# Optimization experiments

Measured on AMD Instinct MI355X. Metric: run time of the kernel, lower is better.

Reference implementation:

```python
import jax, jax.numpy as jnp
import numpy as np
import math

D_MODEL = 1024
EXPAND = 2
D_INNER = D_MODEL * EXPAND          # 2048
D_STATE = 16
NHEADS = 8
NGROUPS = 1
D_CONV = 4
HEADDIM = D_INNER // NHEADS         # 256
CONV_DIM = D_INNER + 2 * NGROUPS * D_STATE   # x, B, C go through the causal conv
D_IN_PROJ = 2 * D_INNER + 2 * NGROUPS * D_STATE + NHEADS  # z, xBC, dt
CHUNK = 64
BATCH = 4
SEQLEN = 4096


def setup_inputs() -> dict:
    key = jax.random.key(0)
    ks = jax.random.split(key, 6)
    rng = np.random.default_rng(0)
    u = jax.random.normal(ks[0], (BATCH, SEQLEN, D_MODEL), dtype=jnp.float32)
    W_in = jax.random.normal(ks[1], (D_MODEL, D_IN_PROJ), dtype=jnp.float32) * 0.02
    conv_w = jax.random.normal(ks[2], (CONV_DIM, D_CONV), dtype=jnp.float32) * (1.0 / math.sqrt(D_CONV))
    conv_b = jnp.zeros((CONV_DIM,), dtype=jnp.float32)
    # dt_bias = inverse-softplus of dt sampled log-uniform in [dt_min, dt_max]
    dt = np.exp(rng.uniform(size=NHEADS) * (math.log(0.1) - math.log(0.001)) + math.log(0.001))
    dt = np.clip(dt, 1e-4, None)
    dt_bias = jnp.asarray(dt + np.log(-np.expm1(-dt)), dtype=jnp.float32)
    # A in A_init_range=(0.9, 0.999), stored as A_log with A = -exp(A_log)
    A_log = jnp.asarray(np.log(rng.uniform(0.9, 0.999, NHEADS)), dtype=jnp.float32)
    D = jnp.ones((NHEADS,), dtype=jnp.float32)
    norm_w = jnp.ones((D_INNER,), dtype=jnp.float32)
    W_out = jax.random.normal(ks[3], (D_INNER, D_MODEL), dtype=jnp.float32) * 0.02
    return {"u": u, "W_in": W_in, "conv_w": conv_w, "conv_b": conv_b,
            "dt_bias": dt_bias, "A_log": A_log, "D": D, "norm_w": norm_w, "W_out": W_out}


def _mamba2_fwd(u, W_in, conv_w, conv_b, dt_bias, A_log, D, norm_w, W_out):
    b, l, _ = u.shape
    h, p, n, g, Q = NHEADS, HEADDIM, D_STATE, NGROUPS, CHUNK
    zxbcdt = u @ W_in                                   # [b,l,2*d_inner+2gn+h]
    z = zxbcdt[..., :D_INNER]
    xBC = zxbcdt[..., D_INNER:D_INNER + CONV_DIM]
    dt = jax.nn.softplus(zxbcdt[..., D_INNER + CONV_DIM:] + dt_bias)  # [b,l,h]
    # causal depthwise conv over time (d_conv taps) + SiLU
    xp = jnp.pad(xBC, ((0, 0), (D_CONV - 1, 0), (0, 0)))
    xconv = conv_b
    for k in range(D_CONV):
        xconv = xconv + xp[:, k:k + l, :] * conv_w[:, k]
    xBC = jax.nn.silu(xconv)
    x = xBC[..., :D_INNER].reshape(b, l, h, p)
    B = xBC[..., D_INNER:D_INNER + g * n].reshape(b, l, g, n)
    C = xBC[..., D_INNER + g * n:].reshape(b, l, g, n)
    Bh = jnp.repeat(B, h // g, axis=2)                  # [b,l,h,n]
    Ch = jnp.repeat(C, h // g, axis=2)
    A = -jnp.exp(A_log)                                 # [h]
    # ---- chunked (SSD) selective scan ----
    nc = l // Q
    xc = x.reshape(b, nc, Q, h, p)
    dtc = dt.reshape(b, nc, Q, h)
    Bc = Bh.reshape(b, nc, Q, h, n)
    Cc = Ch.reshape(b, nc, Q, h, n)
    a = dtc * A                                         # [b,nc,Q,h]
    cs = jnp.cumsum(a, axis=2).transpose(0, 1, 3, 2)    # [b,nc,h,Q]
    mask = jnp.tril(jnp.ones((Q, Q), dtype=bool))
    L = jnp.where(mask, jnp.exp(cs[..., :, None] - cs[..., None, :]), 0.0)  # [b,nc,h,Q,Q]
    xdt = xc * dtc[..., None]                           # x scaled by dt
    Y_diag = jnp.einsum('bcqhn,bcshn,bchqs,bcshp->bcqhp', Cc, Bc, L, xdt)
    decay_states = jnp.exp(cs[..., -1:] - cs)           # [b,nc,h,Q]
    states = jnp.einsum('bcqhn,bchq,bcqhp->bchpn', Bc, decay_states, xdt)  # per-chunk state
    chunk_decay = jnp.exp(cs[..., -1])                  # [b,nc,h]
    def step(carry, inp):
        st, dec = inp
        new = dec[..., None, None] * carry + st
        return new, carry
    init = jnp.zeros((b, h, p, n), dtype=u.dtype)
    _, prev = jax.lax.scan(step, init, (states.transpose(1, 0, 2, 3, 4), chunk_decay.transpose(1, 0, 2)))
    prev = prev.transpose(1, 0, 2, 3, 4)                # state entering each chunk [b,nc,h,p,n]
    Y_off = jnp.einsum('bcqhn,bchpn,bchq->bcqhp', Cc, prev, jnp.exp(cs))
    y = (Y_diag + Y_off).reshape(b, l, h, p) + D[:, None] * x
    y = y.reshape(b, l, D_INNER)
    # gated RMSNorm then out projection
    y = y * jax.nn.silu(z)
    y = y * jax.lax.rsqrt(jnp.mean(y * y, axis=-1, keepdims=True) + 1e-5) * norm_w
    return y @ W_out


def reference(u, W_in, conv_w, conv_b, dt_bias, A_log, D, norm_w, W_out):
    return _mamba2_fwd(u, W_in, conv_w, conv_b, dt_bias, A_log, D, norm_w, W_out)
```

## Files before the change

kernel.cpp:

```cpp
#include <hip/hip_runtime.h>
#include <cstddef>
#include <cstdint>
#include <type_traits>

constexpr int DM = 1024;
constexpr int DI = 2048;
constexpr int DS = 16;
constexpr int NH = 8;
constexpr int CD = 2080;
constexpr int DP = 4136;
constexpr int DPT = 4224;
constexpr int Q  = 64;
constexpr int B_ = 4;
constexpr int L_ = 4096;
constexpr int NCH = 64;
constexpr int HP = 256;
constexpr int NR = B_ * L_;

constexpr size_t AL(size_t x) { return (x + 255) & ~(size_t)255; }
constexpr size_t OFFB_ZX = 0;
constexpr size_t OFFB_BC = AL(OFFB_ZX + (size_t)NR * DP * 2);
constexpr size_t OFFB_DT = AL(OFFB_BC + (size_t)NR * 32 * 4);
constexpr size_t OFFB_CS = AL(OFFB_DT + (size_t)NR * NH * 4);
constexpr size_t OFFB_ST = AL(OFFB_CS + (size_t)B_ * NCH * NH * Q * 4);
constexpr size_t OFFB_Y  = AL(OFFB_ST + (size_t)B_ * NCH * NH * HP * DS * 4);
constexpr size_t OFFB_WO = AL(OFFB_Y + (size_t)NR * DI * 2);

__device__ __forceinline__ float silu_f(float x) { return x / (1.f + expf(-x)); }
__device__ __forceinline__ float bf2f(unsigned short v) {
  unsigned int u = ((unsigned int)v) << 16;
  return __builtin_bit_cast(float, u);
}
__device__ __forceinline__ unsigned short f2bf(float f) {
  unsigned int u = __builtin_bit_cast(unsigned int, f);
  u += 0x7FFFu + ((u >> 16) & 1u);
  return (unsigned short)(u >> 16);
}

typedef __attribute__((ext_vector_type(8))) short bf16x8;
typedef __attribute__((ext_vector_type(4))) float f32x4;

template<bool OUT_BF16>
__global__ __launch_bounds__(256)
void gemm_mfma(const unsigned short* __restrict__ A, const unsigned short* __restrict__ Bt,
               void* __restrict__ Cout, int M, int N, int K, int ldc) {
  __shared__ unsigned short As[128 * 64];
  __shared__ unsigned short Bs[128 * 64];
  const int t = threadIdx.x;
  const int w = t >> 6, l = t & 63;
  const int quad = l >> 4, lan = l & 15;
  const int wm = w >> 1, wn = w & 1;
  const int ncol = gridDim.x;
  const int id = blockIdx.y * ncol + blockIdx.x;
  const int xcd = id & 7, slot = id >> 3;
  const int rpx = gridDim.y >> 3;
  const int row_g = xcd * rpx + slot / ncol;
  const int col_g = slot - (slot / ncol) * ncol;
  const int row0 = row_g * 128, col0 = col_g * 128;

  f32x4 acc[4][4];
  #pragma unroll
  for (int i = 0; i < 4; ++i)
    #pragma unroll
    for (int j = 0; j < 4; ++j)
      acc[i][j] = (f32x4)(0.0f);

  for (int k0 = 0; k0 < K; k0 += 64) {
    __syncthreads();
    #pragma unroll
    for (int i = 0; i < 4; ++i) {
      const int jc = i * 256 + w * 64 + l;
      const int m = jc >> 3, c8 = jc & 7;
      const int gc8 = c8 ^ (m & 7);
      const unsigned short* gp = A + (size_t)(row0 + m) * K + k0 + (gc8 << 3);
      unsigned short* lp = &As[(size_t)(i * 256 + w * 64) * 8];
      __builtin_amdgcn_global_load_lds((const __attribute__((address_space(1))) void*)gp,
                                       (__attribute__((address_space(3))) void*)lp, 16, 0, 0);
    }
    #pragma unroll
    for (int i = 0; i < 4; ++i) {
      const int jc = i * 256 + w * 64 + l;
      const int n = jc >> 3, c8 = jc & 7;
      const int gc8 = c8 ^ (n & 7);
      const unsigned short* gp = Bt + (size_t)(col0 + n) * K + k0 + (gc8 << 3);
      unsigned short* lp = &Bs[(size_t)(i * 256 + w * 64) * 8];
      __builtin_amdgcn_global_load_lds((const __attribute__((address_space(1))) void*)gp,
                                       (__attribute__((address_space(3))) void*)lp, 16, 0, 0);
    }
    __syncthreads();
    #pragma unroll
    for (int kk = 0; kk < 64; kk += 32) {
      const int kc = quad + (kk >> 3);
      bf16x8 af[4], bf[4];
      #pragma unroll
      for (int mi = 0; mi < 4; ++mi) {
        const int m = wm * 64 + mi * 16 + lan;
        af[mi] = *(const bf16x8*)&As[m * 64 + ((kc ^ (m & 7)) << 3)];
      }
      #pragma unroll
      for (int ni = 0; ni < 4; ++ni) {
        const int n = wn * 64 + ni * 16 + lan;
        bf[ni] = *(const bf16x8*)&Bs[n * 64 + ((kc ^ (n & 7)) << 3)];
      }
      #pragma unroll
      for (int mi = 0; mi < 4; ++mi)
        #pragma unroll
        for (int ni = 0; ni < 4; ++ni)
          acc[mi][ni] = __builtin_amdgcn_mfma_f32_16x16x32_bf16(af[mi], bf[ni], acc[mi][ni], 0, 0, 0);
    }
  }
  #pragma unroll
  for (int mi = 0; mi < 4; ++mi) {
    const size_t rb = row0 + wm * 64 + mi * 16 + quad * 4;
    #pragma unroll
    for (int ni = 0; ni < 4; ++ni) {
      const int colb = col0 + wn * 64 + ni * 16 + lan;
      if (colb < N) {
        if constexpr (OUT_BF16) {
          unsigned short* C = (unsigned short*)Cout;
          #pragma unroll
          for (int r = 0; r < 4; ++r)
            C[(rb + r) * (size_t)ldc + colb] = f2bf(acc[mi][ni][r]);
        } else {
          float* C = (float*)Cout;
          #pragma unroll
          for (int r = 0; r < 4; ++r)
            C[(rb + r) * (size_t)ldc + colb] = acc[mi][ni][r];
        }
      }
    }
  }
}

__global__ __launch_bounds__(256)
void cvt_bf16(const float* __restrict__ src, unsigned short* __restrict__ dst, size_t n4) {
  const size_t i = ((size_t)blockIdx.x * 256 + threadIdx.x) * 4;
  if (i < n4 * 4) {
    float4 v = *(const float4*)(src + i);
    ushort4 o;
    o.x = f2bf(v.x); o.y = f2bf(v.y); o.z = f2bf(v.z); o.w = f2bf(v.w);
    *(ushort4*)(dst + i) = o;
  }
}

__global__ __launch_bounds__(256)
void transpose_cvt(const float* __restrict__ src, unsigned short* __restrict__ dst,
                   int R, int C, int Cvalid) {
  __shared__ float T[64][65];
  const int t = threadIdx.x;
  const int n0 = blockIdx.x * 64, k0 = blockIdx.y * 64;
  #pragma unroll
  for (int i = 0; i < 4; ++i) {
    int f = t + i * 256;
    int r = f >> 4, c4 = (f & 15) << 2;
    int n = n0 + c4;
    float4 v = make_float4(0.f, 0.f, 0.f, 0.f);
    if (n + 3 < Cvalid) {
      v = *(const float4*)(src + (size_t)(k0 + r) * C + n);
    } else {
      if (n + 0 < Cvalid) v.x = src[(size_t)(k0 + r) * C + n + 0];
      if (n + 1 < Cvalid) v.y = src[(size_t)(k0 + r) * C + n + 1];
      if (n + 2 < Cvalid) v.z = src[(size_t)(k0 + r) * C + n + 2];
      if (n + 3 < Cvalid) v.w = src[(size_t)(k0 + r) * C + n + 3];
    }
    T[r][c4 + 0] = v.x; T[r][c4 + 1] = v.y; T[r][c4 + 2] = v.z; T[r][c4 + 3] = v.w;
  }
  __syncthreads();
  #pragma unroll
  for (int i = 0; i < 4; ++i) {
    int f = t + i * 256;
    int c = f >> 4, r4 = (f & 15) << 2;
    ushort4 o;
    o.x = f2bf(T[r4 + 0][c]); o.y = f2bf(T[r4 + 1][c]);
    o.z = f2bf(T[r4 + 2][c]); o.w = f2bf(T[r4 + 3][c]);
    *(ushort4*)(dst + (size_t)(n0 + c) * R + k0 + r4) = o;
  }
}

__global__ __launch_bounds__(256)
void convbc_kernel(const unsigned short* __restrict__ zx, const float* __restrict__ cw,
                   const float* __restrict__ cb, float* __restrict__ bc) {
  const int idx = blockIdx.x * 256 + threadIdx.x;
  const int j = idx & 31;
  const int row = idx >> 5;
  const int l = row & (L_ - 1);
  const int cc = DI + j;
  float a = cb[cc];
  #pragma unroll
  for (int k = 0; k < 4; ++k) {
    int ll = l - 3 + k;
    if (ll >= 0)
      a += bf2f(zx[(size_t)(row - 3 + k) * DP + (DI + DI + j)]) * cw[cc * 4 + k];
  }
  bc[(size_t)row * 32 + j] = silu_f(a);
}

__global__ __launch_bounds__(256)
void dt_kernel(const unsigned short* __restrict__ zx, const float* __restrict__ dt_bias,
               float* __restrict__ dt) {
  const int i = blockIdx.x * 256 + threadIdx.x;
  const int h = i & 7;
  const size_t row = (size_t)(i >> 3);
  float x = bf2f(zx[row * DP + (DI + CD) + h]) + dt_bias[h];
  dt[i] = (x > 20.f) ? x : log1pf(expf(x));
}

__global__ __launch_bounds__(256)
void chunk_kernel(const unsigned short* __restrict__ zx, const float* __restrict__ bc,
                  const float* __restrict__ dt, const float* __restrict__ A_log,
                  const float* __restrict__ cw, const float* __restrict__ cb,
                  const float* __restrict__ Dp, float* __restrict__ cs_out,
                  float* __restrict__ states, unsigned short* __restrict__ yb) {
  const int c = blockIdx.x, h = blockIdx.y, b = blockIdx.z;
  const int t = threadIdx.x;
  const int w = t >> 6, l = t & 63;
  const int quad = l >> 4, lan = l & 15;
  __shared__ float dtS[Q], csS[Q], ddS[Q];
  __shared__ float BsS[Q][DS + 1];
  __shared__ __align__(16) unsigned short Msd[Q][Q + 8];
  __shared__ __align__(16) unsigned short BdT[DS][Q + 8];
  __shared__ __align__(16) char regionA[Q * (Q + 8) * 2];
  __shared__ __align__(16) char regionB[Q * DS * 4 + Q * (Q + 8) * 2];
  float (*CsS)[DS]                 = (float(*)[DS])regionA;
  unsigned short (*xsT)[Q + 8]     = (unsigned short(*)[Q + 8])regionA;
  unsigned short (*rawS)[Q]        = (unsigned short(*)[Q])regionB;
  float (*stS)[DS]                 = (float(*)[DS])regionB;
  unsigned short (*ytS)[Q + 8]     = (unsigned short(*)[Q + 8])(regionB + Q * DS * 4);
  const size_t rowb = (size_t)b * L_ + (size_t)c * Q;

  if (t < Q) {
    float dtv = dt[(rowb + t) * NH + h];
    dtS[t] = dtv;
    float s = dtv * (-expf(A_log[h]));
    #pragma unroll
    for (int off = 1; off < 64; off <<= 1) {
      float n = __shfl_up(s, off, 64);
      if (t >= off) s += n;
    }
    csS[t] = s;
    float slast = __shfl(s, 63, 64);
    ddS[t] = expf(slast - s) * dtv;
    cs_out[(((size_t)b * NCH + c) * NH + h) * Q + t] = s;
  }
  for (int i = t; i < Q * DS; i += 256) {
    int q = i >> 4, n = i & 15;
    BsS[q][n] = bc[(rowb + q) * 32 + n];
    CsS[q][n] = bc[(rowb + q) * 32 + 16 + n];
  }
  __syncthreads();
  for (int i = t; i < DS * Q; i += 256) {
    int n = i & 15, q = i >> 4;
    BdT[n][q] = f2bf(BsS[q][n] * ddS[q]);
  }
  const float Dh = Dp[h];
  for (int i = t; i < Q * Q; i += 256) {
    int q = i >> 6, s = i & 63;
    float v = 0.f;
    if (s <= q) {
      float d = 0.f;
      #pragma unroll
      for (int n = 0; n < DS; ++n) d += CsS[q][n] * BsS[s][n];
      v = expf(csS[q] - csS[s]) * d * dtS[s];
      if (s == q) v += Dh;
    }
    Msd[q][s] = f2bf(v);
  }

  const int pch = l;
  uint4 r0 = make_uint4(0, 0, 0, 0), r1 = make_uint4(0, 0, 0, 0), r2 = make_uint4(0, 0, 0, 0);
  {
    const int col0 = DI + h * HP;
    const unsigned short* gb = zx + ((size_t)b * L_ + (c * Q - 3)) * DP + col0;
    if (c > 0 || t >= 24) r0 = *(const uint4*)(gb + (size_t)(t >> 3) * DP + (t & 7) * 8);
    r1 = *(const uint4*)(gb + (size_t)((t + 256) >> 3) * DP + (t & 7) * 8);
    if (t < 24) r2 = *(const uint4*)(gb + (size_t)((t + 512) >> 3) * DP + (t & 7) * 8);
  }

  for (int pt = 0; pt < 4; ++pt) {
    uint4* rw = (uint4*)rawS;
    rw[t] = r0; rw[t + 256] = r1;
    if (t < 24) rw[t + 512] = r2;
    __syncthreads();
    {
      const int cc = h * HP + pt * Q + pch;
      const float w0 = cw[cc * 4 + 0], w1 = cw[cc * 4 + 1];
      const float w2 = cw[cc * 4 + 2], w3 = cw[cc * 4 + 3];
      const float bias = cb[cc];
      const int q0 = w * 16;
      unsigned short ob[16];
      #pragma unroll
      for (int i2 = 0; i2 < 16; ++i2) {
        int q = q0 + i2;
        float a = bias + bf2f(rawS[q][pch]) * w0 + bf2f(rawS[q + 1][pch]) * w1
                       + bf2f(rawS[q + 2][pch]) * w2 + bf2f(rawS[q + 3][pch]) * w3;
        ob[i2] = f2bf(silu_f(a));
      }
      *(uint4*)&xsT[pch][q0 + 0] = *(uint4*)&ob[0];
      *(uint4*)&xsT[pch][q0 + 8] = *(uint4*)&ob[8];
    }
    if (pt < 3) {
      const int col0n = DI + h * HP + (pt + 1) * Q;
      const unsigned short* gb = zx + ((size_t)b * L_ + (c * Q - 3)) * DP + col0n;
      r0 = make_uint4(0, 0, 0, 0); r2 = make_uint4(0, 0, 0, 0);
      if (c > 0 || t >= 24) r0 = *(const uint4*)(gb + (size_t)(t >> 3) * DP + (t & 7) * 8);
      r1 = *(const uint4*)(gb + (size_t)((t + 256) >> 3) * DP + (t & 7) * 8);
      if (t < 24) r2 = *(const uint4*)(gb + (size_t)((t + 512) >> 3) * DP + (t & 7) * 8);
    }
    __syncthreads();
    bf16x8 xfrag[2];
    #pragma unroll
    for (int ks = 0; ks < 2; ++ks)
      xfrag[ks] = *(const bf16x8*)&xsT[w * 16 + lan][quad * 8 + ks * 32];
    {
      f32x4 sacc = (f32x4)(0.0f);
      #pragma unroll
      for (int ks = 0; ks < 2; ++ks) {
        bf16x8 bfr = *(const bf16x8*)&BdT[lan][quad * 8 + ks * 32];
        sacc = __builtin_amdgcn_mfma_f32_16x16x32_bf16(xfrag[ks], bfr, sacc, 0, 0, 0);
      }
      #pragma unroll
      for (int r = 0; r < 4; ++r)
        stS[w * 16 + quad * 4 + r][lan] = sacc[r];
    }
    {
      #pragma unroll
      for (int mi = 0; mi < 4; ++mi) {
        f32x4 yac = (f32x4)(0.0f);
        #pragma unroll
        for (int ks = 0; ks < 2; ++ks) {
          bf16x8 am = *(const bf16x8*)&Msd[mi * 16 + lan][quad * 8 + ks * 32];
          yac = __builtin_amdgcn_mfma_f32_16x16x32_bf16(am, xfrag[ks], yac, 0, 0, 0);
        }
        #pragma unroll
        for (int r = 0; r < 4; ++r)
          ytS[mi * 16 + quad * 4 + r][w * 16 + lan] = f2bf(yac[r]);
      }
    }
    __syncthreads();
    {
      const size_t stbase = ((((size_t)b * NCH + c) * NH + h) * HP + (size_t)pt * Q) * DS;
      ((float4*)(states + stbase))[t] = ((const float4*)&stS[0][0])[t];
    }
    {
      const int colbase = h * HP + pt * Q;
      #pragma unroll
      for (int pass = 0; pass < 2; ++pass) {
        int q = pass * 32 + (t >> 3), p8 = (t & 7) * 8;
        *(uint4*)(yb + (rowb + q) * (size_t)DI + colbase + p8) = *(const uint4*)&ytS[q][p8];
      }
    }
    __syncthreads();
  }
}

__global__ __launch_bounds__(256)
void scan_kernel(float* __restrict__ states, const float* __restrict__ cs) {
  const int pn = blockIdx.x * 256 + threadIdx.x;
  const int h = blockIdx.y, b = blockIdx.z;
  const size_t cstride = (size_t)NH * HP * DS;
  const size_t base = ((size_t)b * NCH * NH + h) * (size_t)(HP * DS) + pn;
  float carry = 0.f;
  for (int c = 0; c < NCH; ++c) {
    float dec = expf(cs[(((size_t)b * NCH + c) * NH + h) * Q + (Q - 1)]);
    float st = states[base + (size_t)c * cstride];
    states[base + (size_t)c * cstride] = carry;
    carry = dec * carry + st;
  }
}

__global__ __launch_bounds__(256)
void yoff_kernel(const float* __restrict__ bc, const float* __restrict__ cs,
                 const float* __restrict__ prev, unsigned short* __restrict__ yb) {
  const int c = blockIdx.x, h = blockIdx.y, b = blockIdx.z;
  const int t = threadIdx.x;
  __shared__ __align__(16) float CsS[Q][DS];
  __shared__ float ecs[Q];
  const size_t rowb = (size_t)b * L_ + (size_t)c * Q;
  const size_t pb = (((size_t)b * NCH + c) * NH + h) * (size_t)(HP * DS);
  for (int i = t; i < Q * DS; i += 256) {
    int q = i >> 4, n = i & 15;
    CsS[q][n] = bc[(rowb + q) * 32 + 16 + n];
  }
  if (t < Q) ecs[t] = expf(cs[(((size_t)b * NCH + c) * NH + h) * Q + t]);
  float pv[16];
  #pragma unroll
  for (int k = 0; k < 4; ++k)
    *(float4*)&pv[k * 4] = *(const float4*)(prev + pb + (size_t)t * DS + k * 4);
  __syncthreads();
  for (int q = 0; q < Q; ++q) {
    float acc = 0.f;
    #pragma unroll
    for (int n = 0; n < DS; ++n) acc += CsS[q][n] * pv[n];
    const size_t idx = (rowb + q) * DI + h * HP + t;
    yb[idx] = f2bf(bf2f(yb[idx]) + ecs[q] * acc);
  }
}

__global__ __launch_bounds__(256)
void gatenorm_kernel(const unsigned short* __restrict__ zx, const float* __restrict__ norm_w,
                     unsigned short* __restrict__ yb) {
  const size_t row = blockIdx.x;
  const int t = threadIdx.x;
  const unsigned short* zrow = zx + row * DP;
  unsigned short* yrow = yb + row * DI;
  const int d0 = t * 8;
  uint4 yv = *(const uint4*)(yrow + d0);
  uint4 zv = *(const uint4*)(zrow + d0);
  const unsigned short* ys = (const unsigned short*)&yv;
  const unsigned short* zs = (const unsigned short*)&zv;
  float v[8];
  float ss = 0.f;
  #pragma unroll
  for (int j = 0; j < 8; ++j) {
    float val = bf2f(ys[j]) * silu_f(bf2f(zs[j]));
    v[j] = val;
    ss += val * val;
  }
  #pragma unroll
  for (int off = 32; off > 0; off >>= 1) ss += __shfl_down(ss, off);
  __shared__ float red[4];
  if ((t & 63) == 0) red[t >> 6] = ss;
  __syncthreads();
  float tot = red[0] + red[1] + red[2] + red[3];
  float scale = rsqrtf(tot / (float)DI + 1e-5f);
  ushort4 o[2];
  unsigned short* op = (unsigned short*)o;
  #pragma unroll
  for (int j = 0; j < 8; ++j) op[j] = f2bf(v[j] * scale * norm_w[d0 + j]);
  *(uint4*)(yrow + d0) = *(uint4*)o;
}

extern "C" void kernel_launch(void* const* d_in, const int* in_sizes, int n_in,
                              void* d_out, int out_size, void* d_ws, size_t ws_size,
                              hipStream_t stream) {
  const float* u       = (const float*)d_in[0];
  const float* W_in    = (const float*)d_in[1];
  const float* conv_w  = (const float*)d_in[2];
  const float* conv_b  = (const float*)d_in[3];
  const float* dt_bias = (const float*)d_in[4];
  const float* A_log   = (const float*)d_in[5];
  const float* Dp      = (const float*)d_in[6];
  const float* norm_w  = (const float*)d_in[7];
  const float* W_out   = (const float*)d_in[8];
  float* out = (float*)d_out;
  char* w = (char*)d_ws;

  unsigned short* zx  = (unsigned short*)(w + OFFB_ZX);
  float* bcb          = (float*)(w + OFFB_BC);
  float* dtb          = (float*)(w + OFFB_DT);
  float* csb          = (float*)(w + OFFB_CS);
  float* stb          = (float*)(w + OFFB_ST);
  unsigned short* yb  = (unsigned short*)(w + OFFB_Y);
  unsigned short* ub  = (unsigned short*)(w + OFFB_ST);
  unsigned short* wib = (unsigned short*)(w + OFFB_Y);
  unsigned short* wob = (unsigned short*)(w + OFFB_WO);

  cvt_bf16<<<(NR * DM / 4 + 255) / 256, 256, 0, stream>>>(u, ub, (size_t)NR * DM / 4);
  transpose_cvt<<<dim3(DPT / 64, DM / 64), 256, 0, stream>>>(W_in, wib, DM, DP, DP);
  transpose_cvt<<<dim3(DM / 64, DI / 64), 256, 0, stream>>>(W_out, wob, DI, DM, DM);
  gemm_mfma<true><<<dim3(DPT / 128, NR / 128), 256, 0, stream>>>(
      ub, wib, zx, NR, DP, DM, DP);
  convbc_kernel<<<(NR * 32) / 256, 256, 0, stream>>>(zx, conv_w, conv_b, bcb);
  dt_kernel<<<(NR * NH) / 256, 256, 0, stream>>>(zx, dt_bias, dtb);
  chunk_kernel<<<dim3(NCH, NH, B_), 256, 0, stream>>>(zx, bcb, dtb, A_log, conv_w,
                                                      conv_b, Dp, csb, stb, yb);
  scan_kernel<<<dim3((HP * DS) / 256, NH, B_), 256, 0, stream>>>(stb, csb);
  yoff_kernel<<<dim3(NCH, NH, B_), 256, 0, stream>>>(bcb, csb, stb, yb);
  gatenorm_kernel<<<NR, 256, 0, stream>>>(zx, norm_w, yb);
  gemm_mfma<false><<<dim3(DM / 128, NR / 128), 256, 0, stream>>>(
      yb, wob, out, NR, DM, DI, DM);
}
```

Measured before the change: 542.8 us.

## Replace GEMM with 256x256-tile, 512-thread kernel using a 4-stage LDS ring

Both projection GEMMs move from 128x128 tiles with a single-buffered K=64 loop to 256x256 tiles with 8 waves. Operand loads go through a 4-slot ring of K=32 slices prefetched three steps ahead with explicit vmcnt waits, and MFMA issue is interleaved with s_setprio. The aim is more reuse per loaded byte and hiding global-load latency behind compute. In exchange it uses more registers and LDS, pads the in_proj N dimension to 4352 (more wasted columns), and launches fewer blocks, which may leave some CUs idle on the smaller out_proj GEMM.

```diff
diff --git a/kernel.cpp b/kernel.cpp
--- a/kernel.cpp
+++ b/kernel.cpp
@@ -1,7 +1,6 @@
 #include <hip/hip_runtime.h>
 #include <cstddef>
 #include <cstdint>
-#include <type_traits>
 
 constexpr int DM = 1024;
 constexpr int DI = 2048;
@@ -9,7 +8,7 @@
 constexpr int NH = 8;
 constexpr int CD = 2080;
 constexpr int DP = 4136;
-constexpr int DPT = 4224;
+constexpr int DPT = 4352;
 constexpr int Q  = 64;
 constexpr int B_ = 4;
 constexpr int L_ = 4096;
@@ -40,96 +39,125 @@
 typedef __attribute__((ext_vector_type(8))) short bf16x8;
 typedef __attribute__((ext_vector_type(4))) float f32x4;
 
+__device__ __forceinline__ void bar() {
+  asm volatile("" ::: "memory");
+  __builtin_amdgcn_s_barrier();
+  asm volatile("" ::: "memory");
+}
+
 template<bool OUT_BF16>
-__global__ __launch_bounds__(256)
-void gemm_mfma(const unsigned short* __restrict__ A, const unsigned short* __restrict__ Bt,
-               void* __restrict__ Cout, int M, int N, int K, int ldc) {
-  __shared__ unsigned short As[128 * 64];
-  __shared__ unsigned short Bs[128 * 64];
+__global__ __launch_bounds__(512, 2)
+void gemm256(const unsigned short* __restrict__ A, const unsigned short* __restrict__ Bt,
+             void* __restrict__ Cout, int M, int N, int K, int ldc) {
+  __shared__ __align__(16) unsigned short ring[4][2][256 * 32];
   const int t = threadIdx.x;
   const int w = t >> 6, l = t & 63;
   const int quad = l >> 4, lan = l & 15;
-  const int wm = w >> 1, wn = w & 1;
+  const int wm = w >> 2, wn = w & 3;
   const int ncol = gridDim.x;
   const int id = blockIdx.y * ncol + blockIdx.x;
-  const int xcd = id & 7, slot = id >> 3;
+  const int xcd = id & 7, slot0 = id >> 3;
   const int rpx = gridDim.y >> 3;
-  const int row_g = xcd * rpx + slot / ncol;
-  const int col_g = slot - (slot / ncol) * ncol;
-  const int row0 = row_g * 128, col0 = col_g * 128;
-
-  f32x4 acc[4][4];
-  #pragma unroll
-  for (int i = 0; i < 4; ++i)
-    #pragma unroll
-    for (int j = 0; j < 4; ++j)
-      acc[i][j] = (f32x4)(0.0f);
-
-  for (int k0 = 0; k0 < K; k0 += 64) {
-    __syncthreads();
-    #pragma unroll
-    for (int i = 0; i < 4; ++i) {
-      const int jc = i * 256 + w * 64 + l;
-      const int m = jc >> 3, c8 = jc & 7;
-      const int gc8 = c8 ^ (m & 7);
-      const unsigned short* gp = A + (size_t)(row0 + m) * K + k0 + (gc8 << 3);
-      unsigned short* lp = &As[(size_t)(i * 256 + w * 64) * 8];
-      __builtin_amdgcn_global_load_lds((const __attribute__((address_space(1))) void*)gp,
-                                       (__attribute__((address_space(3))) void*)lp, 16, 0, 0);
-    }
-    #pragma unroll
-    for (int i = 0; i < 4; ++i) {
-      const int jc = i * 256 + w * 64 + l;
-      const int n = jc >> 3, c8 = jc & 7;
-      const int gc8 = c8 ^ (n & 7);
-      const unsigned short* gp = Bt + (size_t)(col0 + n) * K + k0 + (gc8 << 3);
-      unsigned short* lp = &Bs[(size_t)(i * 256 + w * 64) * 8];
-      __builtin_amdgcn_global_load_lds((const __attribute__((address_space(1))) void*)gp,
-                                       (__attribute__((address_space(3))) void*)lp, 16, 0, 0);
-    }
-    __syncthreads();
-    #pragma unroll
-    for (int kk = 0; kk < 64; kk += 32) {
-      const int kc = quad + (kk >> 3);
-      bf16x8 af[4], bf[4];
-      #pragma unroll
-      for (int mi = 0; mi < 4; ++mi) {
-        const int m = wm * 64 + mi * 16 + lan;
-        af[mi] = *(const bf16x8*)&As[m * 64 + ((kc ^ (m & 7)) << 3)];
-      }
+  const int row_g = xcd * rpx + slot0 / ncol;
+  const int col_g = slot0 - (slot0 / ncol) * ncol;
+  const int row0 = row_g * 256, col0 = col_g * 256;
+
+  const int NSLOT = K >> 5;
+
+  auto stage = [&](int s, int mat) {
+    const int ss = (s < NSLOT) ? s : 0;
+    const unsigned short* G = mat ? Bt : A;
+    const int b0 = mat ? col0 : row0;
+    unsigned short* lb = ring[s & 3][mat];
+    const int k0 = ss << 5;
+    #pragma unroll
+    for (int i = 0; i < 2; ++i) {
+      const int f = i * 512 + t;
+      const int r = f >> 2, c = f & 3;
+      const unsigned short* gp = G + (size_t)(b0 + r) * K + k0 + ((c ^ (r & 3)) << 3);
+      __builtin_amdgcn_global_load_lds(
+          (const __attribute__((address_space(1))) void*)gp,
+          (__attribute__((address_space(3))) void*)(lb + (size_t)f * 8), 16, 0, 0);
+    }
+  };
+
+  f32x4 acc[2][4][4];
+  #pragma unroll
+  for (int rq = 0; rq < 2; ++rq)
+    #pragma unroll
+    for (int mi = 0; mi < 4; ++mi)
+      #pragma unroll
+      for (int ni = 0; ni < 4; ++ni)
+        acc[rq][mi][ni] = (f32x4)(0.0f);
+
+  stage(0, 0); stage(0, 1);
+  stage(1, 0); stage(1, 1);
+  stage(2, 0); stage(2, 1);
+
+  for (int s = 0; s < NSLOT; ++s) {
+    asm volatile("s_waitcnt vmcnt(8)" ::: "memory");
+    bar();
+    const unsigned short* Aslot = ring[s & 3][0];
+    const unsigned short* Bslot = ring[s & 3][1];
+    bf16x8 af[4], bf[4];
+    #pragma unroll
+    for (int ni = 0; ni < 4; ++ni) {
+      const int r = wn * 64 + ni * 16 + lan;
+      bf[ni] = *(const bf16x8*)&Bslot[r * 32 + ((quad ^ (r & 3)) << 3)];
+    }
+    #pragma unroll
+    for (int mi = 0; mi < 4; ++mi) {
+      const int r = wm * 128 + mi * 16 + lan;
+      af[mi] = *(const bf16x8*)&Aslot[r * 32 + ((quad ^ (r & 3)) << 3)];
+    }
+    stage(s + 3, 0);
+    __builtin_amdgcn_s_setprio(1);
+    #pragma unroll
+    for (int mi = 0; mi < 4; ++mi)
+      #pragma unroll
+      for (int ni = 0; ni < 4; ++ni)
+        acc[0][mi][ni] = __builtin_amdgcn_mfma_f32_16x16x32_bf16(af[mi], bf[ni], acc[0][mi][ni], 0, 0, 0);
+    __builtin_amdgcn_s_setprio(0);
+    #pragma unroll
+    for (int mi = 0; mi < 4; ++mi) {
+      const int r = wm * 128 + 64 + mi * 16 + lan;
+      af[mi] = *(const bf16x8*)&Aslot[r * 32 + ((quad ^ (r & 3)) << 3)];
+    }
+    stage(s + 3, 1);
+    __builtin_amdgcn_s_setprio(1);
+    #pragma unroll
+    for (int mi = 0; mi < 4; ++mi)
+      #pragma unroll
+      for (int ni = 0; ni < 4; ++ni)
+        acc[1][mi][ni] = __builtin_amdgcn_mfma_f32_16x16x32_bf16(af[mi], bf[ni], acc[1][mi][ni], 0, 0, 0);
+    __builtin_amdgcn_s_setprio(0);
+    bar();
+  }
+  asm volatile("s_waitcnt vmcnt(0)" ::: "memory");
+
+  #pragma unroll
+  for (int rq = 0; rq < 2; ++rq)
+    #pragma unroll
+    for (int mi = 0; mi < 4; ++mi) {
+      const size_t rb = row0 + wm * 128 + rq * 64 + mi * 16 + quad * 4;
       #pragma unroll
       for (int ni = 0; ni < 4; ++ni) {
-        const int n = wn * 64 + ni * 16 + lan;
-        bf[ni] = *(const bf16x8*)&Bs[n * 64 + ((kc ^ (n & 7)) << 3)];
-      }
-      #pragma unroll
-      for (int mi = 0; mi < 4; ++mi)
-        #pragma unroll
-        for (int ni = 0; ni < 4; ++ni)
-          acc[mi][ni] = __builtin_amdgcn_mfma_f32_16x16x32_bf16(af[mi], bf[ni], acc[mi][ni], 0, 0, 0);
-    }
-  }
-  #pragma unroll
-  for (int mi = 0; mi < 4; ++mi) {
-    const size_t rb = row0 + wm * 64 + mi * 16 + quad * 4;
-    #pragma unroll
-    for (int ni = 0; ni < 4; ++ni) {
-      const int colb = col0 + wn * 64 + ni * 16 + lan;
-      if (colb < N) {
-        if constexpr (OUT_BF16) {
-          unsigned short* C = (unsigned short*)Cout;
-          #pragma unroll
-          for (int r = 0; r < 4; ++r)
-            C[(rb + r) * (size_t)ldc + colb] = f2bf(acc[mi][ni][r]);
-        } else {
-          float* C = (float*)Cout;
-          #pragma unroll
-          for (int r = 0; r < 4; ++r)
-            C[(rb + r) * (size_t)ldc + colb] = acc[mi][ni][r];
+        const int colb = col0 + wn * 64 + ni * 16 + lan;
+        if (colb < N) {
+          if constexpr (OUT_BF16) {
+            unsigned short* C = (unsigned short*)Cout;
+            #pragma unroll
+            for (int r = 0; r < 4; ++r)
+              C[(rb + r) * (size_t)ldc + colb] = f2bf(acc[rq][mi][ni][r]);
+          } else {
+            float* C = (float*)Cout;
+            #pragma unroll
+            for (int r = 0; r < 4; ++r)
+              C[(rb + r) * (size_t)ldc + colb] = acc[rq][mi][ni][r];
+          }
         }
       }
     }
-  }
 }
 
 __global__ __launch_bounds__(256)
@@ -458,7 +486,7 @@
   cvt_bf16<<<(NR * DM / 4 + 255) / 256, 256, 0, stream>>>(u, ub, (size_t)NR * DM / 4);
   transpose_cvt<<<dim3(DPT / 64, DM / 64), 256, 0, stream>>>(W_in, wib, DM, DP, DP);
   transpose_cvt<<<dim3(DM / 64, DI / 64), 256, 0, stream>>>(W_out, wob, DI, DM, DM);
-  gemm_mfma<true><<<dim3(DPT / 128, NR / 128), 256, 0, stream>>>(
+  gemm256<true><<<dim3(DPT / 256, NR / 256), 512, 0, stream>>>(
       ub, wib, zx, NR, DP, DM, DP);
   convbc_kernel<<<(NR * 32) / 256, 256, 0, stream>>>(zx, conv_w, conv_b, bcb);
   dt_kernel<<<(NR * NH) / 256, 256, 0, stream>>>(zx, dt_bias, dtb);
@@ -467,6 +495,6 @@
   scan_kernel<<<dim3((HP * DS) / 256, NH, B_), 256, 0, stream>>>(stb, csb);
   yoff_kernel<<<dim3(NCH, NH, B_), 256, 0, stream>>>(bcb, csb, stb, yb);
   gatenorm_kernel<<<NR, 256, 0, stream>>>(zx, norm_w, yb);
-  gemm_mfma<false><<<dim3(DM / 128, NR / 128), 256, 0, stream>>>(
+  gemm256<false><<<dim3(DM / 256, NR / 256), 512, 0, stream>>>(
       yb, wob, out, NR, DM, DI, DM);
 }
```

Result: no change. 536.9 us (-1.1%).
